# Kernel optimization log

Hardware: AMD Instinct MI355X
Metric: run time of the kernel (lower is better)

The kernel has to match this reference:

```python
import jax, jax.numpy as jnp
import numpy as np

N_HEADS = 16
EMBED = 1024
SEQ = 2048
BATCH = 4
GELU_C = 0.044715
EPS = 1e-5


def gelu_tanh(x):
    return 0.5 * x * (1.0 + jnp.tanh(jnp.sqrt(2.0 / jnp.pi) * (x + GELU_C * x ** 3)))


def layer_norm(x, scale, shift):
    mean = jnp.mean(x, axis=-1, keepdims=True)
    var = jnp.var(x, axis=-1, keepdims=True)
    return scale * (x - mean) / jnp.sqrt(var + EPS) + shift


def setup_inputs() -> dict:
    key = jax.random.key(0)
    ks = jax.random.split(key, 8)
    d = EMBED
    s = 0.02
    return {
        "X": jax.random.normal(ks[0], (BATCH, SEQ, d), dtype=jnp.float32),
        "Wq": jax.random.normal(ks[1], (d, d), dtype=jnp.float32) * s,
        "Wk": jax.random.normal(ks[2], (d, d), dtype=jnp.float32) * s,
        "Wv": jax.random.normal(ks[3], (d, d), dtype=jnp.float32) * s,
        "Wo": jax.random.normal(ks[4], (d, d), dtype=jnp.float32) * s,
        "W1": jax.random.normal(ks[5], (d, 4 * d), dtype=jnp.float32) * s,
        "b1": jnp.zeros((4 * d,), dtype=jnp.float32),
        "W2": jax.random.normal(ks[6], (4 * d, d), dtype=jnp.float32) * s,
        "b2": jnp.zeros((d,), dtype=jnp.float32),
        "ln1_scale": jnp.ones((d,), dtype=jnp.float32),
        "ln1_shift": jnp.zeros((d,), dtype=jnp.float32),
        "ln2_scale": jnp.ones((d,), dtype=jnp.float32),
        "ln2_shift": jnp.zeros((d,), dtype=jnp.float32),
    }


def attention(x, Wq, Wk, Wv, Wo):
    b, s, d = x.shape
    h, dh = N_HEADS, d // N_HEADS
    q = (x @ Wq).reshape(b, s, h, dh).transpose(0, 2, 1, 3)  # [b,h,s,dh]
    k = (x @ Wk).reshape(b, s, h, dh).transpose(0, 2, 1, 3)
    v = (x @ Wv).reshape(b, s, h, dh).transpose(0, 2, 1, 3)
    scores = jnp.einsum("bhqd,bhkd->bhqk", q, k) / jnp.sqrt(jnp.float32(dh))
    causal = jnp.tril(jnp.ones((s, s), dtype=bool))
    scores = jnp.where(causal, scores, -jnp.inf)
    w = jax.nn.softmax(scores, axis=-1)  # dropout rate 0 -> identity
    ctx = jnp.einsum("bhqk,bhkd->bhqd", w, v)
    ctx = ctx.transpose(0, 2, 1, 3).reshape(b, s, d)
    return ctx @ Wo


def reference(X, Wq, Wk, Wv, Wo, W1, b1, W2, b2,
              ln1_scale, ln1_shift, ln2_scale, ln2_shift):
    h = layer_norm(X, ln1_scale, ln1_shift)
    X = X + attention(h, Wq, Wk, Wv, Wo)
    h = layer_norm(X, ln2_scale, ln2_shift)
    h = gelu_tanh(h @ W1 + b1) @ W2 + b2
    return X + h
```

## Files before the change

### kernel.cpp

```cpp
#include <hip/hip_runtime.h>

typedef unsigned short u16;
typedef __attribute__((ext_vector_type(8))) short bf16x8;
typedef __attribute__((ext_vector_type(4))) float fx4;

#define MFMA16(a, b, c) __builtin_amdgcn_mfma_f32_16x16x32_bf16((a), (b), (c), 0, 0, 0)

__device__ __forceinline__ u16 f2bf(float f) {
  unsigned u = __float_as_uint(f);
  u += 0x7fffu + ((u >> 16) & 1u);
  return (u16)(u >> 16);
}

__device__ __forceinline__ void gload_lds16(const void* g, void* l) {
  __builtin_amdgcn_global_load_lds((const __attribute__((address_space(1))) void*)g,
                                   (__attribute__((address_space(3))) void*)l,
                                   16, 0, 0);
}

__global__ __launch_bounds__(256) void tcvt(const float* __restrict__ src,
                                            u16* __restrict__ dst, int R, int C) {
  __shared__ float t[32][33];
  const int tx = threadIdx.x & 31, ty = threadIdx.x >> 5;
  const int bx = blockIdx.x, by = blockIdx.y;
#pragma unroll
  for (int i = 0; i < 4; ++i)
    t[ty + i * 8][tx] = src[(size_t)(by * 32 + ty + i * 8) * C + bx * 32 + tx];
  __syncthreads();
#pragma unroll
  for (int i = 0; i < 4; ++i)
    dst[(size_t)(bx * 32 + ty + i * 8) * R + by * 32 + tx] = f2bf(t[tx][ty + i * 8]);
}

__global__ __launch_bounds__(256) void ln_kernel(const float* __restrict__ x,
                                                 const float* __restrict__ sc,
                                                 const float* __restrict__ sh,
                                                 u16* __restrict__ out) {
  const int row = blockIdx.x, tid = threadIdx.x;
  const float4 v = ((const float4*)(x + (size_t)row * 1024))[tid];
  float s = v.x + v.y + v.z + v.w;
  float ss = v.x * v.x + v.y * v.y + v.z * v.z + v.w * v.w;
#pragma unroll
  for (int d = 32; d >= 1; d >>= 1) {
    s += __shfl_xor(s, d);
    ss += __shfl_xor(ss, d);
  }
  __shared__ float rs[4], rq[4];
  const int w = tid >> 6;
  if ((tid & 63) == 0) { rs[w] = s; rq[w] = ss; }
  __syncthreads();
  s = rs[0] + rs[1] + rs[2] + rs[3];
  ss = rq[0] + rq[1] + rq[2] + rq[3];
  const float mean = s * (1.f / 1024.f);
  const float var = ss * (1.f / 1024.f) - mean * mean;
  const float rstd = rsqrtf(var + 1e-5f);
  const float4 g = ((const float4*)sc)[tid];
  const float4 b = ((const float4*)sh)[tid];
  ushort4 o;
  o.x = f2bf(g.x * (v.x - mean) * rstd + b.x);
  o.y = f2bf(g.y * (v.y - mean) * rstd + b.y);
  o.z = f2bf(g.z * (v.z - mean) * rstd + b.z);
  o.w = f2bf(g.w * (v.w - mean) * rstd + b.w);
  ((ushort4*)(out + (size_t)row * 1024))[tid] = o;
}

template <int MODE>
__global__ __launch_bounds__(256) void gemm_bf16(
    const u16* __restrict__ A, const u16* __restrict__ Bt, int M, int N, int K,
    void* __restrict__ outp, const float* __restrict__ aux,
    u16* __restrict__ qd, u16* __restrict__ kd, u16* __restrict__ vd) {
  __shared__ u16 lA[128 * 32];
  __shared__ u16 lB[128 * 32];
  const int tid = threadIdx.x;
  const int w = tid >> 6, lane = tid & 63;
  const int lo = lane & 15, hi = lane >> 4;
  const int tM = blockIdx.y * 128, tN = blockIdx.x * 128;
  const int wr = (w >> 1) << 6, wc = (w & 1) << 6;

  const u16 *sA[2], *sB[2];
  u16 *dA[2], *dB[2];
#pragma unroll
  for (int p = 0; p < 2; ++p) {
    const int c = p * 256 + tid;
    const int r = c >> 2, gs = (c & 3) ^ (r & 3);
    sA[p] = A + (size_t)(tM + r) * K + gs * 8;
    sB[p] = Bt + (size_t)(tN + r) * K + gs * 8;
    dA[p] = &lA[(p * 256 + w * 64) * 8];
    dB[p] = &lB[(p * 256 + w * 64) * 8];
  }

  fx4 acc[4][4];
#pragma unroll
  for (int m = 0; m < 4; ++m)
#pragma unroll
    for (int n = 0; n < 4; ++n) acc[m][n] = (fx4){0.f, 0.f, 0.f, 0.f};

  for (int kk = 0; kk < K; kk += 32) {
    __syncthreads();
#pragma unroll
    for (int p = 0; p < 2; ++p) {
      gload_lds16(sA[p] + kk, dA[p]);
      gload_lds16(sB[p] + kk, dB[p]);
    }
    __syncthreads();
    bf16x8 af[4], bfr[4];
#pragma unroll
    for (int m = 0; m < 4; ++m) {
      const int r = wr + m * 16 + lo;
      af[m] = *(const bf16x8*)&lA[r * 32 + ((hi ^ (r & 3)) << 3)];
    }
#pragma unroll
    for (int n = 0; n < 4; ++n) {
      const int r = wc + n * 16 + lo;
      bfr[n] = *(const bf16x8*)&lB[r * 32 + ((hi ^ (r & 3)) << 3)];
    }
#pragma unroll
    for (int m = 0; m < 4; ++m)
#pragma unroll
      for (int n = 0; n < 4; ++n) acc[m][n] = MFMA16(af[m], bfr[n], acc[m][n]);
  }

#pragma unroll
  for (int m = 0; m < 4; ++m) {
    const int rgb = tM + wr + m * 16 + hi * 4;
#pragma unroll
    for (int n = 0; n < 4; ++n) {
      const int cg = tN + wc + n * 16 + lo;
#pragma unroll
      for (int r = 0; r < 4; ++r) {
        const float v = acc[m][n][r];
        const int rg = rgb + r;
        if constexpr (MODE == 1) {
          float* o = (float*)outp;
          const size_t idx = (size_t)rg * 1024 + cg;
          o[idx] = aux[idx] + v;
        } else {
          float* o = (float*)outp;
          const size_t idx = (size_t)rg * 1024 + cg;
          o[idx] = o[idx] + v + aux[cg];
        }
      }
    }
  }
}

template <int MODE>
__global__ __launch_bounds__(512, 1) void gemm256(
    const u16* __restrict__ A, const u16* __restrict__ Bt, int K,
    void* __restrict__ outp, const float* __restrict__ aux,
    u16* __restrict__ qd, u16* __restrict__ kd, u16* __restrict__ vd) {
  __shared__ u16 lds[2][2][256 * 64];
  const int tid = threadIdx.x;
  const int lane = tid & 63, w = tid >> 6;
  const int lo = lane & 15, hi = lane >> 4;
  const int wm = w >> 2, wn = w & 3;
  const int tM = blockIdx.y * 256, tN = blockIdx.x * 256;
  const int NT = K >> 6;

  const int rb = tid >> 3;
  const int uc = ((tid & 7) ^ (rb & 7)) * 8;

#define STGH(BUFI, XI, XPTR, TOFF, H, KK)                                        \
  do {                                                                           \
    _Pragma("unroll") for (int ph = 0; ph < 2; ++ph) {                           \
      const int rl = (H) * 128 + ph * 64 + rb;                                   \
      gload_lds16(XPTR + (size_t)((TOFF) + rl) * K + (KK) + uc,                  \
                  &lds[BUFI][XI][(H) * 8192 + ph * 4096 + tid * 8]);             \
    }                                                                            \
  } while (0)

  fx4 acc[8][4];
#pragma unroll
  for (int m = 0; m < 8; ++m)
#pragma unroll
    for (int n = 0; n < 4; ++n) acc[m][n] = (fx4){0.f, 0.f, 0.f, 0.f};

#pragma unroll
  for (int pt = 0; pt < 2; ++pt) {
    STGH(pt, 0, A, tM, 0, pt * 64);
    STGH(pt, 0, A, tM, 1, pt * 64);
    STGH(pt, 1, Bt, tN, 0, pt * 64);
    STGH(pt, 1, Bt, tN, 1, pt * 64);
  }

  for (int t = 0; t < NT; ++t) {
    const int bi = t & 1;
    const u16* bufA = &lds[bi][0][0];
    const u16* bufB = &lds[bi][1][0];
    if (t == NT - 1) {
      asm volatile("s_waitcnt vmcnt(0)" ::: "memory");
    } else {
      asm volatile("s_waitcnt vmcnt(8)" ::: "memory");
    }
    __builtin_amdgcn_s_barrier();

    bf16x8 bfr[4][2], afr[4][2];
#pragma unroll
    for (int n = 0; n < 4; ++n)
#pragma unroll
      for (int ks = 0; ks < 2; ++ks) {
        const int R = wn * 64 + n * 16 + lo;
        bfr[n][ks] = *(const bf16x8*)&bufB[R * 64 + (((ks << 2) + hi) ^ (R & 7)) * 8];
      }
#pragma unroll
    for (int m = 0; m < 4; ++m)
#pragma unroll
      for (int ks = 0; ks < 2; ++ks) {
        const int R = wm * 128 + m * 16 + lo;
        afr[m][ks] = *(const bf16x8*)&bufA[R * 64 + (((ks << 2) + hi) ^ (R & 7)) * 8];
      }
    asm volatile("s_waitcnt lgkmcnt(0)" ::: "memory");
    __builtin_amdgcn_sched_barrier(0);
    __builtin_amdgcn_s_barrier();
    if (t + 2 < NT) {
      STGH(bi, 1, Bt, tN, 0, (t + 2) * 64);
      STGH(bi, 1, Bt, tN, 1, (t + 2) * 64);
    }
    bf16x8 afr2[4][2];
#pragma unroll
    for (int m = 0; m < 4; ++m)
#pragma unroll
      for (int ks = 0; ks < 2; ++ks) {
        const int R = wm * 128 + (m + 4) * 16 + lo;
        afr2[m][ks] = *(const bf16x8*)&bufA[R * 64 + (((ks << 2) + hi) ^ (R & 7)) * 8];
      }
    __builtin_amdgcn_s_setprio(1);
#pragma unroll
    for (int m = 0; m < 4; ++m)
#pragma unroll
      for (int n = 0; n < 4; ++n) {
        acc[m][n] = MFMA16(afr[m][0], bfr[n][0], acc[m][n]);
        acc[m][n] = MFMA16(afr[m][1], bfr[n][1], acc[m][n]);
      }
    __builtin_amdgcn_s_setprio(0);
    asm volatile("s_waitcnt lgkmcnt(0)" ::: "memory");
    __builtin_amdgcn_sched_barrier(0);
    __builtin_amdgcn_s_barrier();
    if (t + 2 < NT) {
      STGH(bi, 0, A, tM, 0, (t + 2) * 64);
      STGH(bi, 0, A, tM, 1, (t + 2) * 64);
    }
    __builtin_amdgcn_s_setprio(1);
#pragma unroll
    for (int m = 0; m < 4; ++m)
#pragma unroll
      for (int n = 0; n < 4; ++n) {
        acc[m + 4][n] = MFMA16(afr2[m][0], bfr[n][0], acc[m + 4][n]);
        acc[m + 4][n] = MFMA16(afr2[m][1], bfr[n][1], acc[m + 4][n]);
      }
    __builtin_amdgcn_s_setprio(0);
  }
#undef STGH

#pragma unroll
  for (int m = 0; m < 8; ++m) {
    const int rgb = tM + wm * 128 + m * 16 + hi * 4;
#pragma unroll
    for (int n = 0; n < 4; ++n) {
      const int cg = tN + wn * 64 + n * 16 + lo;
#pragma unroll
      for (int r = 0; r < 4; ++r) {
        const float v = acc[m][n][r];
        const int rg = rgb + r;
        if constexpr (MODE == 0) {
          const int which = cg >> 10, c = cg & 1023;
          const int head = c >> 6, dhi = c & 63;
          const int b = rg >> 11, sidx = rg & 2047;
          const int bh = b * 16 + head;
          const u16 bv = f2bf(v);
          if (which == 0)      qd[((size_t)bh * 2048 + sidx) * 64 + dhi] = bv;
          else if (which == 1) kd[((size_t)bh * 2048 + sidx) * 64 + dhi] = bv;
          else                 vd[((size_t)bh * 64 + dhi) * 2048 + sidx] = bv;
        } else {
          const float xx = v + aux[cg];
          const float t2 = xx + 0.044715f * xx * xx * xx;
          const float e = __expf(1.5957691216057308f * t2);
          const float th = 1.f - 2.f / (e + 1.f);
          ((u16*)outp)[(size_t)rg * 4096 + cg] = f2bf(0.5f * xx * (1.f + th));
        }
      }
    }
  }
}

__global__ __launch_bounds__(512) void attn_kernel(const u16* __restrict__ Q,
                                                   const u16* __restrict__ Kg,
                                                   const u16* __restrict__ Vt,
                                                   u16* __restrict__ ctx) {
  __shared__ u16 lK[2][64 * 64];
  __shared__ u16 lV[2][64 * 64];
  __shared__ u16 Plds[8][16 * 64];
  const int tid = threadIdx.x;
  const int w = tid >> 6, lane = tid & 63;
  const int lo = lane & 15, hi = lane >> 4;
  const int bh = blockIdx.x;
  const int j = blockIdx.y;
  const u16* Qb = Q + (size_t)bh * 2048 * 64;
  const u16* Kb = Kg + (size_t)bh * 2048 * 64;
  const u16* Vb = Vt + (size_t)bh * 64 * 2048;
  u16* Pw = Plds[w];
  const int nt0 = 2 * j + 2;

  const int rowS = tid >> 3;
  const int ugS = (tid & 7) ^ (rowS & 7);

#define STAGE(BUF, KB)                                                         \
  do {                                                                         \
    gload_lds16(Kb + (size_t)((KB) + rowS) * 64 + ugS * 8, &lK[BUF][tid * 8]); \
    gload_lds16(Vb + (size_t)rowS * 2048 + (KB) + ugS * 8, &lV[BUF][tid * 8]); \
  } while (0)

  const int b = bh >> 4, h = bh & 15;
  const float SCALE = 0.18033688011112042f;

  int qt = j;
  int qw = qt * 128 + w * 16;

  bf16x8 qf[2];
#pragma unroll
  for (int kc = 0; kc < 2; ++kc)
    qf[kc] = *(const bf16x8*)&Qb[(size_t)(qw + lo) * 64 + kc * 32 + hi * 8];

  fx4 accO[4];
  float mrow[4], lrow[4];
#pragma unroll
  for (int t2 = 0; t2 < 4; ++t2) {
    accO[t2] = (fx4){0.f, 0.f, 0.f, 0.f};
    mrow[t2] = -1e30f;
    lrow[t2] = 0.f;
  }

  STAGE(0, 0);
  __syncthreads();

  int buf = 0;
  for (int t = 0; t < 34; ++t) {
    if (t + 1 < 34) {
      const int tn = t + 1;
      const int kbn = (tn < nt0 ? tn : tn - nt0) * 64;
      STAGE(buf ^ 1, kbn);
    }
    if (t == nt0) {
#pragma unroll
      for (int t2 = 0; t2 < 4; ++t2)
#pragma unroll
        for (int r = 0; r < 4; ++r) {
          const int rg = b * 2048 + qw + hi * 4 + r;
          const int cg = h * 64 + t2 * 16 + lo;
          ctx[(size_t)rg * 1024 + cg] = f2bf(accO[t2][r] / lrow[r]);
        }
      qt = 15 - j;
      qw = qt * 128 + w * 16;
#pragma unroll
      for (int kc = 0; kc < 2; ++kc)
        qf[kc] = *(const bf16x8*)&Qb[(size_t)(qw + lo) * 64 + kc * 32 + hi * 8];
#pragma unroll
      for (int t2 = 0; t2 < 4; ++t2) {
        accO[t2] = (fx4){0.f, 0.f, 0.f, 0.f};
        mrow[t2] = -1e30f;
        lrow[t2] = 0.f;
      }
    }
    const int kb = (t < nt0 ? t : t - nt0) * 64;
    if (kb <= qw + 15) {
      const u16* lKb = lK[buf];
      const u16* lVb = lV[buf];
      fx4 s[4];
#pragma unroll
      for (int tt = 0; tt < 4; ++tt) {
        const int r = tt * 16 + lo;
        const bf16x8 kf0 = *(const bf16x8*)&lKb[r * 64 + ((hi ^ (r & 7)) << 3)];
        const bf16x8 kf1 = *(const bf16x8*)&lKb[r * 64 + (((4 + hi) ^ (r & 7)) << 3)];
        fx4 z = (fx4){0.f, 0.f, 0.f, 0.f};
        z = MFMA16(qf[0], kf0, z);
        z = MFMA16(qf[1], kf1, z);
        s[tt] = z;
      }
      if (kb + 63 > qw) {
#pragma unroll
        for (int tt = 0; tt < 4; ++tt)
#pragma unroll
          for (int r = 0; r < 4; ++r) {
            const int key = kb + tt * 16 + lo;
            const int qr = qw + hi * 4 + r;
            s[tt][r] = (key > qr) ? -1e30f : s[tt][r] * SCALE;
          }
      } else {
#pragma unroll
        for (int tt = 0; tt < 4; ++tt)
#pragma unroll
          for (int r = 0; r < 4; ++r) s[tt][r] *= SCALE;
      }
      float mt[4];
#pragma unroll
      for (int r = 0; r < 4; ++r)
        mt[r] = fmaxf(fmaxf(s[0][r], s[1][r]), fmaxf(s[2][r], s[3][r]));
#pragma unroll
      for (int d = 8; d >= 1; d >>= 1)
#pragma unroll
        for (int r = 0; r < 4; ++r) mt[r] = fmaxf(mt[r], __shfl_xor(mt[r], d));
      bool ok = true;
#pragma unroll
      for (int r = 0; r < 4; ++r) ok = ok && (mt[r] <= mrow[r] + 8.f);
      if (!__all(ok)) {
#pragma unroll
        for (int r = 0; r < 4; ++r) {
          const float mn = fmaxf(mrow[r], mt[r]);
          const float fsc = exp2f(mrow[r] - mn);
          mrow[r] = mn;
          lrow[r] *= fsc;
#pragma unroll
          for (int t2 = 0; t2 < 4; ++t2) accO[t2][r] *= fsc;
        }
      }
      float la[4] = {0.f, 0.f, 0.f, 0.f};
#pragma unroll
      for (int tt = 0; tt < 4; ++tt)
#pragma unroll
        for (int r = 0; r < 4; ++r) {
          const float p = exp2f(s[tt][r] - mrow[r]);
          s[tt][r] = p;
          la[r] += p;
        }
#pragma unroll
      for (int d = 8; d >= 1; d >>= 1)
#pragma unroll
        for (int r = 0; r < 4; ++r) la[r] += __shfl_xor(la[r], d);
#pragma unroll
      for (int r = 0; r < 4; ++r) lrow[r] += la[r];
#pragma unroll
      for (int tt = 0; tt < 4; ++tt)
#pragma unroll
        for (int r = 0; r < 4; ++r) {
          const int row = hi * 4 + r;
          const int colB = (tt * 16 + lo) * 2;
          Pw[(row * 128 + (colB ^ ((row & 7) << 4))) >> 1] = f2bf(s[tt][r]);
        }
      asm volatile("s_waitcnt lgkmcnt(0)" ::: "memory");
      bf16x8 pf[2];
#pragma unroll
      for (int kc = 0; kc < 2; ++kc) {
        const int row = lo;
        const int colB = kc * 64 + hi * 16;
        pf[kc] = *(const bf16x8*)((const char*)Pw + row * 128 + (colB ^ ((row & 7) << 4)));
      }
#pragma unroll
      for (int t2 = 0; t2 < 4; ++t2) {
        const int r2 = t2 * 16 + lo;
        const bf16x8 vf0 = *(const bf16x8*)&lVb[r2 * 64 + ((hi ^ (r2 & 7)) << 3)];
        const bf16x8 vf1 = *(const bf16x8*)&lVb[r2 * 64 + (((4 + hi) ^ (r2 & 7)) << 3)];
        accO[t2] = MFMA16(pf[0], vf0, accO[t2]);
        accO[t2] = MFMA16(pf[1], vf1, accO[t2]);
      }
    }
    __syncthreads();
    buf ^= 1;
  }
#pragma unroll
  for (int t2 = 0; t2 < 4; ++t2)
#pragma unroll
    for (int r = 0; r < 4; ++r) {
      const int rg = b * 2048 + qw + hi * 4 + r;
      const int cg = h * 64 + t2 * 16 + lo;
      ctx[(size_t)rg * 1024 + cg] = f2bf(accO[t2][r] / lrow[r]);
    }
#undef STAGE
}

extern "C" void kernel_launch(void* const* d_in, const int* in_sizes, int n_in,
                              void* d_out, int out_size, void* d_ws, size_t ws_size,
                              hipStream_t stream) {
  const float* X    = (const float*)d_in[0];
  const float* Wq   = (const float*)d_in[1];
  const float* Wk   = (const float*)d_in[2];
  const float* Wv   = (const float*)d_in[3];
  const float* Wo   = (const float*)d_in[4];
  const float* W1   = (const float*)d_in[5];
  const float* b1   = (const float*)d_in[6];
  const float* W2   = (const float*)d_in[7];
  const float* b2   = (const float*)d_in[8];
  const float* ln1s = (const float*)d_in[9];
  const float* ln1b = (const float*)d_in[10];
  const float* ln2s = (const float*)d_in[11];
  const float* ln2b = (const float*)d_in[12];

  const size_t SZ_WQKVT = 3072UL * 1024;
  const size_t SZ_WOT   = 1024UL * 1024;
  const size_t SZ_W1T   = 4096UL * 1024;
  const size_t SZ_W2T   = 1024UL * 4096;
  const size_t SZ_H     = 8192UL * 1024;
  const size_t SZ_QKV   = 64UL * 2048 * 64;

  u16* WqkvT = (u16*)d_ws;
  u16* WoT   = WqkvT + SZ_WQKVT;
  u16* W1T   = WoT + SZ_WOT;
  u16* W2T   = W1T + SZ_W1T;
  u16* hbuf  = W2T + SZ_W2T;
  u16* qbuf  = hbuf + SZ_H;
  u16* kbuf  = qbuf + SZ_QKV;
  u16* vbuf  = kbuf + SZ_QKV;
  u16* gbuf  = vbuf + SZ_QKV;
  u16* ctx   = hbuf;
  u16* h2    = qbuf;

  float* out = (float*)d_out;
  dim3 blk(256);

  tcvt<<<dim3(32, 32), blk, 0, stream>>>(Wq, WqkvT, 1024, 1024);
  tcvt<<<dim3(32, 32), blk, 0, stream>>>(Wk, WqkvT + 1024 * 1024, 1024, 1024);
  tcvt<<<dim3(32, 32), blk, 0, stream>>>(Wv, WqkvT + 2 * 1024 * 1024, 1024, 1024);
  tcvt<<<dim3(32, 32), blk, 0, stream>>>(Wo, WoT, 1024, 1024);
  tcvt<<<dim3(128, 32), blk, 0, stream>>>(W1, W1T, 1024, 4096);
  tcvt<<<dim3(32, 128), blk, 0, stream>>>(W2, W2T, 4096, 1024);

  ln_kernel<<<8192, blk, 0, stream>>>(X, ln1s, ln1b, hbuf);
  gemm256<0><<<dim3(12, 32), dim3(512), 0, stream>>>(hbuf, WqkvT, 1024,
                                                     nullptr, nullptr, qbuf, kbuf, vbuf);
  attn_kernel<<<dim3(64, 8), dim3(512), 0, stream>>>(qbuf, kbuf, vbuf, ctx);
  gemm_bf16<1><<<dim3(8, 64), blk, 0, stream>>>(ctx, WoT, 8192, 1024, 1024,
                                                out, X, nullptr, nullptr, nullptr);
  ln_kernel<<<8192, blk, 0, stream>>>(out, ln2s, ln2b, h2);
  gemm256<2><<<dim3(16, 32), dim3(512), 0, stream>>>(h2, W1T, 1024,
                                                     gbuf, b1, nullptr, nullptr, nullptr);
  gemm_bf16<3><<<dim3(8, 64), blk, 0, stream>>>(gbuf, W2T, 8192, 1024, 4096,
                                                out, b2, nullptr, nullptr, nullptr);
}
```

Measured before the change: 480.8 us.

## Replace 128x128 GEMMs with pipelined 256x128 kernel and merge weight conversions

Swaps the simple single-buffered 128x128 bf16 GEMM used for the output projection and the second MLP matmul for a 256x128 tile kernel. The new kernel double-buffers K-slices of 64 in LDS, prefetches two stages ahead with explicit waitcnt and barriers, and raises wave priority around the MFMA blocks. It also folds the six weight transpose/convert launches into one launch that picks its source matrix from the block index. The aim is to hide global-load latency and get more reuse per tile, at the cost of more LDS per block and occupancy limited to one block per CU.

```diff
diff --git a/kernel.cpp b/kernel.cpp
--- a/kernel.cpp
+++ b/kernel.cpp
@@ -18,11 +18,30 @@
                                    16, 0, 0);
 }
 
-__global__ __launch_bounds__(256) void tcvt(const float* __restrict__ src,
-                                            u16* __restrict__ dst, int R, int C) {
+struct WP {
+  const float* s[6];
+  u16* d[6];
+};
+__global__ __launch_bounds__(256) void tcvt_all(WP p) {
   __shared__ float t[32][33];
+  const int id = blockIdx.x;
+  int which, bx, by, R, C;
+  if (id < 4096) {
+    which = id >> 10;
+    const int q = id & 1023;
+    bx = q >> 5; by = q & 31; R = 1024; C = 1024;
+  } else if (id < 8192) {
+    which = 4;
+    const int q = id - 4096;
+    bx = q & 127; by = q >> 7; R = 1024; C = 4096;
+  } else {
+    which = 5;
+    const int q = id - 8192;
+    bx = q & 31; by = q >> 5; R = 4096; C = 1024;
+  }
+  const float* src = p.s[which];
+  u16* dst = p.d[which];
   const int tx = threadIdx.x & 31, ty = threadIdx.x >> 5;
-  const int bx = blockIdx.x, by = blockIdx.y;
 #pragma unroll
   for (int i = 0; i < 4; ++i)
     t[ty + i * 8][tx] = src[(size_t)(by * 32 + ty + i * 8) * C + bx * 32 + tx];
@@ -62,86 +81,6 @@
   o.z = f2bf(g.z * (v.z - mean) * rstd + b.z);
   o.w = f2bf(g.w * (v.w - mean) * rstd + b.w);
   ((ushort4*)(out + (size_t)row * 1024))[tid] = o;
-}
-
-template <int MODE>
-__global__ __launch_bounds__(256) void gemm_bf16(
-    const u16* __restrict__ A, const u16* __restrict__ Bt, int M, int N, int K,
-    void* __restrict__ outp, const float* __restrict__ aux,
-    u16* __restrict__ qd, u16* __restrict__ kd, u16* __restrict__ vd) {
-  __shared__ u16 lA[128 * 32];
-  __shared__ u16 lB[128 * 32];
-  const int tid = threadIdx.x;
-  const int w = tid >> 6, lane = tid & 63;
-  const int lo = lane & 15, hi = lane >> 4;
-  const int tM = blockIdx.y * 128, tN = blockIdx.x * 128;
-  const int wr = (w >> 1) << 6, wc = (w & 1) << 6;
-
-  const u16 *sA[2], *sB[2];
-  u16 *dA[2], *dB[2];
-#pragma unroll
-  for (int p = 0; p < 2; ++p) {
-    const int c = p * 256 + tid;
-    const int r = c >> 2, gs = (c & 3) ^ (r & 3);
-    sA[p] = A + (size_t)(tM + r) * K + gs * 8;
-    sB[p] = Bt + (size_t)(tN + r) * K + gs * 8;
-    dA[p] = &lA[(p * 256 + w * 64) * 8];
-    dB[p] = &lB[(p * 256 + w * 64) * 8];
-  }
-
-  fx4 acc[4][4];
-#pragma unroll
-  for (int m = 0; m < 4; ++m)
-#pragma unroll
-    for (int n = 0; n < 4; ++n) acc[m][n] = (fx4){0.f, 0.f, 0.f, 0.f};
-
-  for (int kk = 0; kk < K; kk += 32) {
-    __syncthreads();
-#pragma unroll
-    for (int p = 0; p < 2; ++p) {
-      gload_lds16(sA[p] + kk, dA[p]);
-      gload_lds16(sB[p] + kk, dB[p]);
-    }
-    __syncthreads();
-    bf16x8 af[4], bfr[4];
-#pragma unroll
-    for (int m = 0; m < 4; ++m) {
-      const int r = wr + m * 16 + lo;
-      af[m] = *(const bf16x8*)&lA[r * 32 + ((hi ^ (r & 3)) << 3)];
-    }
-#pragma unroll
-    for (int n = 0; n < 4; ++n) {
-      const int r = wc + n * 16 + lo;
-      bfr[n] = *(const bf16x8*)&lB[r * 32 + ((hi ^ (r & 3)) << 3)];
-    }
-#pragma unroll
-    for (int m = 0; m < 4; ++m)
-#pragma unroll
-      for (int n = 0; n < 4; ++n) acc[m][n] = MFMA16(af[m], bfr[n], acc[m][n]);
-  }
-
-#pragma unroll
-  for (int m = 0; m < 4; ++m) {
-    const int rgb = tM + wr + m * 16 + hi * 4;
-#pragma unroll
-    for (int n = 0; n < 4; ++n) {
-      const int cg = tN + wc + n * 16 + lo;
-#pragma unroll
-      for (int r = 0; r < 4; ++r) {
-        const float v = acc[m][n][r];
-        const int rg = rgb + r;
-        if constexpr (MODE == 1) {
-          float* o = (float*)outp;
-          const size_t idx = (size_t)rg * 1024 + cg;
-          o[idx] = aux[idx] + v;
-        } else {
-          float* o = (float*)outp;
-          const size_t idx = (size_t)rg * 1024 + cg;
-          o[idx] = o[idx] + v + aux[cg];
-        }
-      }
-    }
-  }
 }
 
 template <int MODE>
@@ -283,6 +222,133 @@
   }
 }
 
+template <int MODE>
+__global__ __launch_bounds__(512, 1) void gemm256x128(
+    const u16* __restrict__ A, const u16* __restrict__ Bt, int K,
+    float* __restrict__ outp, const float* __restrict__ aux) {
+  __shared__ u16 lA[2][256 * 64];
+  __shared__ u16 lB[2][128 * 64];
+  const int tid = threadIdx.x;
+  const int lane = tid & 63, w = tid >> 6;
+  const int lo = lane & 15, hi = lane >> 4;
+  const int wm = w >> 1, wn = w & 1;
+  const int tM = blockIdx.y * 256, tN = blockIdx.x * 128;
+  const int NT = K >> 6;
+
+  const int rb = tid >> 3;
+  const int uc = ((tid & 7) ^ (rb & 7)) * 8;
+
+#define STGA(BUFI, KK)                                                  \
+  do {                                                                  \
+    _Pragma("unroll") for (int i = 0; i < 4; ++i) {                     \
+      gload_lds16(A + (size_t)(tM + i * 64 + rb) * K + (KK) + uc,       \
+                  &lA[BUFI][i * 4096 + tid * 8]);                       \
+    }                                                                   \
+  } while (0)
+#define STGB(BUFI, KK)                                                  \
+  do {                                                                  \
+    _Pragma("unroll") for (int i = 0; i < 2; ++i) {                     \
+      gload_lds16(Bt + (size_t)(tN + i * 64 + rb) * K + (KK) + uc,      \
+                  &lB[BUFI][i * 4096 + tid * 8]);                       \
+    }                                                                   \
+  } while (0)
+
+  fx4 acc[4][4];
+#pragma unroll
+  for (int m = 0; m < 4; ++m)
+#pragma unroll
+    for (int n = 0; n < 4; ++n) acc[m][n] = (fx4){0.f, 0.f, 0.f, 0.f};
+
+  STGA(0, 0);
+  STGB(0, 0);
+  STGA(1, 64);
+  STGB(1, 64);
+
+  for (int t = 0; t < NT; ++t) {
+    const int bi = t & 1;
+    const u16* bufA = &lA[bi][0];
+    const u16* bufB = &lB[bi][0];
+    if (t == NT - 1) {
+      asm volatile("s_waitcnt vmcnt(0)" ::: "memory");
+    } else {
+      asm volatile("s_waitcnt vmcnt(6)" ::: "memory");
+    }
+    __builtin_amdgcn_s_barrier();
+
+    bf16x8 bfr[4][2], af1[2][2];
+#pragma unroll
+    for (int n = 0; n < 4; ++n)
+#pragma unroll
+      for (int ks = 0; ks < 2; ++ks) {
+        const int R = wn * 64 + n * 16 + lo;
+        bfr[n][ks] = *(const bf16x8*)&bufB[R * 64 + (((ks << 2) + hi) ^ (R & 7)) * 8];
+      }
+#pragma unroll
+    for (int m = 0; m < 2; ++m)
+#pragma unroll
+      for (int ks = 0; ks < 2; ++ks) {
+        const int R = wm * 64 + m * 16 + lo;
+        af1[m][ks] = *(const bf16x8*)&bufA[R * 64 + (((ks << 2) + hi) ^ (R & 7)) * 8];
+      }
+    asm volatile("s_waitcnt lgkmcnt(0)" ::: "memory");
+    __builtin_amdgcn_sched_barrier(0);
+    __builtin_amdgcn_s_barrier();
+    if (t + 2 < NT) STGB(bi, (t + 2) * 64);
+    bf16x8 af2[2][2];
+#pragma unroll
+    for (int m = 0; m < 2; ++m)
+#pragma unroll
+      for (int ks = 0; ks < 2; ++ks) {
+        const int R = wm * 64 + (m + 2) * 16 + lo;
+        af2[m][ks] = *(const bf16x8*)&bufA[R * 64 + (((ks << 2) + hi) ^ (R & 7)) * 8];
+      }
+    __builtin_amdgcn_s_setprio(1);
+#pragma unroll
+    for (int m = 0; m < 2; ++m)
+#pragma unroll
+      for (int n = 0; n < 4; ++n) {
+        acc[m][n] = MFMA16(af1[m][0], bfr[n][0], acc[m][n]);
+        acc[m][n] = MFMA16(af1[m][1], bfr[n][1], acc[m][n]);
+      }
+    __builtin_amdgcn_s_setprio(0);
+    asm volatile("s_waitcnt lgkmcnt(0)" ::: "memory");
+    __builtin_amdgcn_sched_barrier(0);
+    __builtin_amdgcn_s_barrier();
+    if (t + 2 < NT) STGA(bi, (t + 2) * 64);
+    __builtin_amdgcn_s_setprio(1);
+#pragma unroll
+    for (int m = 0; m < 2; ++m)
+#pragma unroll
+      for (int n = 0; n < 4; ++n) {
+        acc[m + 2][n] = MFMA16(af2[m][0], bfr[n][0], acc[m + 2][n]);
+        acc[m + 2][n] = MFMA16(af2[m][1], bfr[n][1], acc[m + 2][n]);
+      }
+    __builtin_amdgcn_s_setprio(0);
+  }
+#undef STGA
+#undef STGB
+
+#pragma unroll
+  for (int m = 0; m < 4; ++m) {
+    const int rgb = tM + wm * 64 + m * 16 + hi * 4;
+#pragma unroll
+    for (int n = 0; n < 4; ++n) {
+      const int cg = tN + wn * 64 + n * 16 + lo;
+#pragma unroll
+      for (int r = 0; r < 4; ++r) {
+        const float v = acc[m][n][r];
+        const int rg = rgb + r;
+        const size_t idx = (size_t)rg * 1024 + cg;
+        if constexpr (MODE == 1) {
+          outp[idx] = aux[idx] + v;
+        } else {
+          outp[idx] = outp[idx] + v + aux[cg];
+        }
+      }
+    }
+  }
+}
+
 __global__ __launch_bounds__(512) void attn_kernel(const u16* __restrict__ Q,
                                                    const u16* __restrict__ Kg,
                                                    const u16* __restrict__ Vt,
@@ -506,22 +572,23 @@
   float* out = (float*)d_out;
   dim3 blk(256);
 
-  tcvt<<<dim3(32, 32), blk, 0, stream>>>(Wq, WqkvT, 1024, 1024);
-  tcvt<<<dim3(32, 32), blk, 0, stream>>>(Wk, WqkvT + 1024 * 1024, 1024, 1024);
-  tcvt<<<dim3(32, 32), blk, 0, stream>>>(Wv, WqkvT + 2 * 1024 * 1024, 1024, 1024);
-  tcvt<<<dim3(32, 32), blk, 0, stream>>>(Wo, WoT, 1024, 1024);
-  tcvt<<<dim3(128, 32), blk, 0, stream>>>(W1, W1T, 1024, 4096);
-  tcvt<<<dim3(32, 128), blk, 0, stream>>>(W2, W2T, 4096, 1024);
+  WP wp;
+  wp.s[0] = Wq; wp.s[1] = Wk; wp.s[2] = Wv; wp.s[3] = Wo; wp.s[4] = W1; wp.s[5] = W2;
+  wp.d[0] = WqkvT;
+  wp.d[1] = WqkvT + 1024 * 1024;
+  wp.d[2] = WqkvT + 2 * 1024 * 1024;
+  wp.d[3] = WoT;
+  wp.d[4] = W1T;
+  wp.d[5] = W2T;
+  tcvt_all<<<12288, blk, 0, stream>>>(wp);
 
   ln_kernel<<<8192, blk, 0, stream>>>(X, ln1s, ln1b, hbuf);
   gemm256<0><<<dim3(12, 32), dim3(512), 0, stream>>>(hbuf, WqkvT, 1024,
                                                      nullptr, nullptr, qbuf, kbuf, vbuf);
   attn_kernel<<<dim3(64, 8), dim3(512), 0, stream>>>(qbuf, kbuf, vbuf, ctx);
-  gemm_bf16<1><<<dim3(8, 64), blk, 0, stream>>>(ctx, WoT, 8192, 1024, 1024,
-                                                out, X, nullptr, nullptr, nullptr);
+  gemm256x128<1><<<dim3(8, 32), dim3(512), 0, stream>>>(ctx, WoT, 1024, out, X);
   ln_kernel<<<8192, blk, 0, stream>>>(out, ln2s, ln2b, h2);
   gemm256<2><<<dim3(16, 32), dim3(512), 0, stream>>>(h2, W1T, 1024,
                                                      gbuf, b1, nullptr, nullptr, nullptr);
-  gemm_bf16<3><<<dim3(8, 64), blk, 0, stream>>>(gbuf, W2T, 8192, 1024, 4096,
-                                                out, b2, nullptr, nullptr, nullptr);
-}
+  gemm256x128<3><<<dim3(8, 32), dim3(512), 0, stream>>>(gbuf, W2T, 4096, out, b2);
+}
```

Measured after the change: 489.6 us. About the same (+1.8%).
